# Performance work log

Measured on AMD Instinct MI355X. Metric: run time of the kernel, lower is better.

## Reference

```python
import jax, jax.numpy as jnp
import numpy as np

N = 8192
INITIAL_K = 1.5
SPARSE_WEIGHT = 0.01


def setup_inputs() -> dict:
    key = jax.random.key(0)
    k1, k2, k3 = jax.random.split(key, 3)
    phases = jax.random.normal(k1, (N,), dtype=jnp.float32)
    alive_mask = jax.random.uniform(k2, (N,), dtype=jnp.float32)
    dist_mask = jax.random.uniform(k3, (N, N), dtype=jnp.float32)
    K = jnp.full((N, N), INITIAL_K, dtype=jnp.float32)  # torch.full((n,n), initial_k)
    return {"phases": phases, "alive_mask": alive_mask, "dist_mask": dist_mask, "K": K}


def reference(phases, alive_mask, dist_mask, K):
    # phase_diff[i, j] = phases[j] - phases[i]
    phase_diff = phases[None, :] - phases[:, None]            # [N, N]
    effective_mask = (alive_mask[:, None] * alive_mask[None, :]) * dist_mask  # [N, N]
    coupling = jnp.sum(K * effective_mask * jnp.sin(phase_diff), axis=1)      # [N]
    cos_sum = jnp.mean(jnp.cos(phases))
    sin_sum = jnp.mean(jnp.sin(phases))
    R = jnp.sqrt(cos_sum ** 2 + sin_sum ** 2)
    loss = 1.0 - R + 0.01 * jnp.sqrt(jnp.sum(K * K)) + SPARSE_WEIGHT * jnp.sum(jnp.abs(K))
    dtheta = coupling
    return (R, dtheta, loss)
```

## Files before the change

kernel.cpp:

```cpp
#include <hip/hip_runtime.h>
#include <math.h>

#define NN 8192
#define SPARSE_WEIGHT 0.01f


__device__ __forceinline__ float wave_reduce_sum(float v) {
#pragma unroll
    for (int off = 32; off > 0; off >>= 1)
        v += __shfl_down(v, off, 64);
    return v;
}

__global__ __launch_bounds__(256) void prep_kernel(
        const float* __restrict__ phases,
        const float* __restrict__ alive,
        float* __restrict__ sj,
        float* __restrict__ cj,
        float* __restrict__ acc) {
    int j = blockIdx.x * blockDim.x + threadIdx.x;
    float s = 0.f, c = 0.f;
    if (j < NN) {
        float p = phases[j];
        s = sinf(p);
        c = cosf(p);
        float a = alive[j];
        sj[j] = a * s;
        cj[j] = a * c;
    }
    float ws = wave_reduce_sum(s);
    float wc = wave_reduce_sum(c);
    __shared__ float red_s[4], red_c[4];
    int lane = threadIdx.x & 63;
    int wave = threadIdx.x >> 6;
    if (lane == 0) { red_s[wave] = ws; red_c[wave] = wc; }
    __syncthreads();
    if (threadIdx.x == 0) {
        float bs = red_s[0] + red_s[1] + red_s[2] + red_s[3];
        float bc = red_c[0] + red_c[1] + red_c[2] + red_c[3];
        atomicAdd(&acc[1], bs);
        atomicAdd(&acc[0], bc);
    }
}

__global__ __launch_bounds__(256) void row_kernel(
        const float* __restrict__ K,
        const float* __restrict__ dist,
        const float* __restrict__ sj,
        const float* __restrict__ cj,
        const float* __restrict__ phases,
        const float* __restrict__ alive,
        float* __restrict__ dtheta,
        float* __restrict__ pk2,
        float* __restrict__ pka) {
    const int i = blockIdx.x;
    const float4* __restrict__ Kr = (const float4*)(K + (size_t)i * NN);
    const float4* __restrict__ Dr = (const float4*)(dist + (size_t)i * NN);
    const float4* __restrict__ S4 = (const float4*)sj;
    const float4* __restrict__ C4 = (const float4*)cj;

    float t1 = 0.f, t2 = 0.f, k2 = 0.f, ka = 0.f;
#pragma unroll 4
    for (int q = threadIdx.x; q < NN / 4; q += 256) {
        float4 k = Kr[q];
        float4 d = Dr[q];
        float4 s = S4[q];
        float4 c = C4[q];
        float km;
        km = k.x * d.x; t1 += km * s.x; t2 += km * c.x; k2 += k.x * k.x; ka += fabsf(k.x);
        km = k.y * d.y; t1 += km * s.y; t2 += km * c.y; k2 += k.y * k.y; ka += fabsf(k.y);
        km = k.z * d.z; t1 += km * s.z; t2 += km * c.z; k2 += k.z * k.z; ka += fabsf(k.z);
        km = k.w * d.w; t1 += km * s.w; t2 += km * c.w; k2 += k.w * k.w; ka += fabsf(k.w);
    }

    t1 = wave_reduce_sum(t1);
    t2 = wave_reduce_sum(t2);
    k2 = wave_reduce_sum(k2);
    ka = wave_reduce_sum(ka);

    __shared__ float red[4][4];
    int lane = threadIdx.x & 63;
    int wave = threadIdx.x >> 6;
    if (lane == 0) { red[0][wave] = t1; red[1][wave] = t2; red[2][wave] = k2; red[3][wave] = ka; }
    __syncthreads();
    if (threadIdx.x == 0) {
        t1 = red[0][0] + red[0][1] + red[0][2] + red[0][3];
        t2 = red[1][0] + red[1][1] + red[1][2] + red[1][3];
        k2 = red[2][0] + red[2][1] + red[2][2] + red[2][3];
        ka = red[3][0] + red[3][1] + red[3][2] + red[3][3];
        float p = phases[i];
        dtheta[i] = alive[i] * (cosf(p) * t1 - sinf(p) * t2);
        pk2[i] = k2;
        pka[i] = ka;
    }
}

__global__ __launch_bounds__(1024) void finalize_kernel(
        const float* __restrict__ acc,
        const float* __restrict__ pk2,
        const float* __restrict__ pka,
        float* __restrict__ out) {
    float k2 = 0.f, ka = 0.f;
    for (int j = threadIdx.x; j < NN; j += 1024) {
        k2 += pk2[j];
        ka += pka[j];
    }
    k2 = wave_reduce_sum(k2);
    ka = wave_reduce_sum(ka);
    __shared__ float rk2[16], rka[16];
    int lane = threadIdx.x & 63;
    int wave = threadIdx.x >> 6;
    if (lane == 0) { rk2[wave] = k2; rka[wave] = ka; }
    __syncthreads();
    if (threadIdx.x == 0) {
        float sk2 = 0.f, ska = 0.f;
#pragma unroll
        for (int w = 0; w < 16; ++w) { sk2 += rk2[w]; ska += rka[w]; }
        float cs = acc[0] / (float)NN;
        float ss = acc[1] / (float)NN;
        float R = sqrtf(cs * cs + ss * ss);
        out[0] = R;
        out[NN + 1] = 1.0f - R + 0.01f * sqrtf(sk2) + SPARSE_WEIGHT * ska;
    }
}

extern "C" void kernel_launch(void* const* d_in, const int* in_sizes, int n_in,
                              void* d_out, int out_size, void* d_ws, size_t ws_size,
                              hipStream_t stream) {
    const float* phases = (const float*)d_in[0];
    const float* alive  = (const float*)d_in[1];
    const float* dist   = (const float*)d_in[2];
    const float* K      = (const float*)d_in[3];
    float* out = (float*)d_out;
    float* ws  = (float*)d_ws;

    float* acc = ws;
    float* sj  = ws + 4;
    float* cj  = ws + 4 + NN;
    float* pk2 = ws + 4 + 2 * NN;
    float* pka = ws + 4 + 3 * NN;

    (void)hipMemsetAsync(acc, 0, 4 * sizeof(float), stream);

    prep_kernel<<<NN / 256, 256, 0, stream>>>(phases, alive, sj, cj, acc);
    row_kernel<<<NN, 256, 0, stream>>>(K, dist, sj, cj, phases, alive, out + 1, pk2, pka);
    finalize_kernel<<<1, 1024, 0, stream>>>(acc, pk2, pka, out);
}
```

Baseline: 515.2 us.

## Tile coupling reduction into 32-row by 1024-column blocks with atomic row accumulation

```diff
diff --git a/kernel.cpp b/kernel.cpp
--- a/kernel.cpp
+++ b/kernel.cpp
@@ -3,6 +3,8 @@
 
 #define NN 8192
 #define SPARSE_WEIGHT 0.01f
+#define ROWS 32
+#define CT4 256
 
 
 __device__ __forceinline__ float wave_reduce_sum(float v) {
@@ -36,86 +38,91 @@
     if (lane == 0) { red_s[wave] = ws; red_c[wave] = wc; }
     __syncthreads();
     if (threadIdx.x == 0) {
-        float bs = red_s[0] + red_s[1] + red_s[2] + red_s[3];
-        float bc = red_c[0] + red_c[1] + red_c[2] + red_c[3];
-        atomicAdd(&acc[1], bs);
-        atomicAdd(&acc[0], bc);
+        atomicAdd(&acc[1], red_s[0] + red_s[1] + red_s[2] + red_s[3]);
+        atomicAdd(&acc[0], red_c[0] + red_c[1] + red_c[2] + red_c[3]);
     }
 }
 
-__global__ __launch_bounds__(256) void row_kernel(
+__global__ __launch_bounds__(256, 8) void tile_kernel(
         const float* __restrict__ K,
         const float* __restrict__ dist,
         const float* __restrict__ sj,
         const float* __restrict__ cj,
-        const float* __restrict__ phases,
-        const float* __restrict__ alive,
         float* __restrict__ dtheta,
         float* __restrict__ pk2,
         float* __restrict__ pka) {
-    const int i = blockIdx.x;
-    const float4* __restrict__ Kr = (const float4*)(K + (size_t)i * NN);
-    const float4* __restrict__ Dr = (const float4*)(dist + (size_t)i * NN);
-    const float4* __restrict__ S4 = (const float4*)sj;
-    const float4* __restrict__ C4 = (const float4*)cj;
+    const int tid = threadIdx.x;
+    const int tx = blockIdx.x;
+    const int ty = blockIdx.y;
+    const int row_base = ty * ROWS;
+    const int col4 = tx * CT4 + tid;
 
-    float t1 = 0.f, t2 = 0.f, k2 = 0.f, ka = 0.f;
+    const float4* __restrict__ K4 = (const float4*)K;
+    const float4* __restrict__ D4 = (const float4*)dist;
+
+    const float4 s4 = ((const float4*)sj)[col4];
+    const float4 c4 = ((const float4*)cj)[col4];
+
+    __shared__ float red[ROWS][4][2];
+    __shared__ float redk[4][2];
+
+    const int lane = tid & 63;
+    const int wave = tid >> 6;
+
+    float k2 = 0.f, ka = 0.f;
+    size_t idx = (size_t)row_base * (NN / 4) + col4;
+
 #pragma unroll 4
-    for (int q = threadIdx.x; q < NN / 4; q += 256) {
-        float4 k = Kr[q];
-        float4 d = Dr[q];
-        float4 s = S4[q];
-        float4 c = C4[q];
-        float km;
-        km = k.x * d.x; t1 += km * s.x; t2 += km * c.x; k2 += k.x * k.x; ka += fabsf(k.x);
-        km = k.y * d.y; t1 += km * s.y; t2 += km * c.y; k2 += k.y * k.y; ka += fabsf(k.y);
-        km = k.z * d.z; t1 += km * s.z; t2 += km * c.z; k2 += k.z * k.z; ka += fabsf(k.z);
-        km = k.w * d.w; t1 += km * s.w; t2 += km * c.w; k2 += k.w * k.w; ka += fabsf(k.w);
+    for (int r = 0; r < ROWS; ++r, idx += NN / 4) {
+        float4 k = K4[idx];
+        float4 d = D4[idx];
+        float t1, t2, km;
+        km = k.x * d.x; t1  = km * s4.x; t2  = km * c4.x; k2 += k.x * k.x; ka += fabsf(k.x);
+        km = k.y * d.y; t1 += km * s4.y; t2 += km * c4.y; k2 += k.y * k.y; ka += fabsf(k.y);
+        km = k.z * d.z; t1 += km * s4.z; t2 += km * c4.z; k2 += k.z * k.z; ka += fabsf(k.z);
+        km = k.w * d.w; t1 += km * s4.w; t2 += km * c4.w; k2 += k.w * k.w; ka += fabsf(k.w);
+        t1 = wave_reduce_sum(t1);
+        t2 = wave_reduce_sum(t2);
+        if (lane == 0) { red[r][wave][0] = t1; red[r][wave][1] = t2; }
     }
 
-    t1 = wave_reduce_sum(t1);
-    t2 = wave_reduce_sum(t2);
     k2 = wave_reduce_sum(k2);
     ka = wave_reduce_sum(ka);
+    if (lane == 0) { redk[wave][0] = k2; redk[wave][1] = ka; }
+    __syncthreads();
 
-    __shared__ float red[4][4];
-    int lane = threadIdx.x & 63;
-    int wave = threadIdx.x >> 6;
-    if (lane == 0) { red[0][wave] = t1; red[1][wave] = t2; red[2][wave] = k2; red[3][wave] = ka; }
-    __syncthreads();
-    if (threadIdx.x == 0) {
-        t1 = red[0][0] + red[0][1] + red[0][2] + red[0][3];
-        t2 = red[1][0] + red[1][1] + red[1][2] + red[1][3];
-        k2 = red[2][0] + red[2][1] + red[2][2] + red[2][3];
-        ka = red[3][0] + red[3][1] + red[3][2] + red[3][3];
-        float p = phases[i];
-        dtheta[i] = alive[i] * (cosf(p) * t1 - sinf(p) * t2);
-        pk2[i] = k2;
-        pka[i] = ka;
+    if (tid < ROWS) {
+        float t1 = red[tid][0][0] + red[tid][1][0] + red[tid][2][0] + red[tid][3][0];
+        float t2 = red[tid][0][1] + red[tid][1][1] + red[tid][2][1] + red[tid][3][1];
+        int i = row_base + tid;
+        atomicAdd(&dtheta[i], cj[i] * t1 - sj[i] * t2);
+    } else if (tid == ROWS) {
+        int bid = ty * 8 + tx;
+        pk2[bid] = redk[0][0] + redk[1][0] + redk[2][0] + redk[3][0];
+        pka[bid] = redk[0][1] + redk[1][1] + redk[2][1] + redk[3][1];
     }
 }
 
-__global__ __launch_bounds__(1024) void finalize_kernel(
+__global__ __launch_bounds__(256) void finalize_kernel(
         const float* __restrict__ acc,
         const float* __restrict__ pk2,
         const float* __restrict__ pka,
         float* __restrict__ out) {
     float k2 = 0.f, ka = 0.f;
-    for (int j = threadIdx.x; j < NN; j += 1024) {
+    for (int j = threadIdx.x; j < 2048; j += 256) {
         k2 += pk2[j];
         ka += pka[j];
     }
     k2 = wave_reduce_sum(k2);
     ka = wave_reduce_sum(ka);
-    __shared__ float rk2[16], rka[16];
+    __shared__ float rk2[4], rka[4];
     int lane = threadIdx.x & 63;
     int wave = threadIdx.x >> 6;
     if (lane == 0) { rk2[wave] = k2; rka[wave] = ka; }
     __syncthreads();
     if (threadIdx.x == 0) {
-        float sk2 = 0.f, ska = 0.f;
-#pragma unroll
-        for (int w = 0; w < 16; ++w) { sk2 += rk2[w]; ska += rka[w]; }
+        float sk2 = rk2[0] + rk2[1] + rk2[2] + rk2[3];
+        float ska = rka[0] + rka[1] + rka[2] + rka[3];
         float cs = acc[0] / (float)NN;
         float ss = acc[1] / (float)NN;
         float R = sqrtf(cs * cs + ss * ss);
@@ -138,11 +145,13 @@
     float* sj  = ws + 4;
     float* cj  = ws + 4 + NN;
     float* pk2 = ws + 4 + 2 * NN;
-    float* pka = ws + 4 + 3 * NN;
+    float* pka = pk2 + 2048;
 
     (void)hipMemsetAsync(acc, 0, 4 * sizeof(float), stream);
+    (void)hipMemsetAsync(out, 0, (NN + 2) * sizeof(float), stream);
 
     prep_kernel<<<NN / 256, 256, 0, stream>>>(phases, alive, sj, cj, acc);
-    row_kernel<<<NN, 256, 0, stream>>>(K, dist, sj, cj, phases, alive, out + 1, pk2, pka);
-    finalize_kernel<<<1, 1024, 0, stream>>>(acc, pk2, pka, out);
+    dim3 grid(8, NN / ROWS);
+    tile_kernel<<<grid, 256, 0, stream>>>(K, dist, sj, cj, out + 1, pk2, pka);
+    finalize_kernel<<<1, 256, 0, stream>>>(acc, pk2, pka, out);
 }
```

Result: slower. 529.1 us (+2.7%).
